# Performance work log

Measured on AMD Instinct MI355X. Metric: run time of the kernel, lower is better.

## Reference

```python
import jax, jax.numpy as jnp
import numpy as np

B, T, F, D, NL, V = 16, 1024, 80, 512, 3, 28


def _ln(x, g, b, eps=1e-5):
    m = jnp.mean(x, axis=-1, keepdims=True)
    v = jnp.mean((x - m) ** 2, axis=-1, keepdims=True)
    return (x - m) * jax.lax.rsqrt(v + eps) * g + b


def _sru_layer(x, W, wc, bias, g, beta):
    # x: [T, B, din]; W: [din, k*d] (k=4 when din != d, else k=3)
    d = wc.shape[0] // 2
    xn = _ln(x, g, beta)                       # layer_norm=True: LN on layer input
    U = jnp.einsum('tbi,ij->tbj', xn, W)       # [T, B, k*d]
    u0, u1, u2 = U[..., :d], U[..., d:2 * d], U[..., 2 * d:3 * d]
    xres = U[..., 3 * d:4 * d] if W.shape[1] == 4 * d else x  # highway input
    vf, vr = wc[:d], wc[d:]
    bf, br = bias[:d], bias[d:]

    def step(c, inp):
        a0, a1, a2, xr = inp
        f = jax.nn.sigmoid(a1 + vf * c + bf)
        r = jax.nn.sigmoid(a2 + vr * c + br)
        c2 = f * c + (1.0 - f) * a0
        h = r * c2 + (1.0 - r) * xr
        return c2, h

    c0 = jnp.zeros((x.shape[1], d), x.dtype)
    _, h = jax.lax.scan(step, c0, (u0, u1, u2, xres))
    return h


def _lstm_layer(x, wih, whh, bih, bhh):
    # x: [T, B, d]; torch gate order i, f, g, o
    d = whh.shape[1]
    gx = jnp.einsum('tbi,gi->tbg', x, wih) + bih + bhh  # precompute input gates

    def step(carry, gxt):
        h, c = carry
        gts = gxt + h @ whh.T
        i, f, gg, o = jnp.split(gts, 4, axis=-1)
        c2 = jax.nn.sigmoid(f) * c + jax.nn.sigmoid(i) * jnp.tanh(gg)
        h2 = jax.nn.sigmoid(o) * jnp.tanh(c2)
        return (h2, c2), h2

    nb = x.shape[1]
    init = (jnp.zeros((nb, d), x.dtype), jnp.zeros((nb, d), x.dtype))
    _, h = jax.lax.scan(step, init, gx)
    return h


def _forward(x, sru_w0, sru_wc0, sru_b0, sru_ln0_g, sru_ln0_b,
             sru_w, sru_wc, sru_b, sru_ln_g, sru_ln_b,
             lstm_ln_g, lstm_ln_b, lstm_wih, lstm_whh, lstm_bih, lstm_bhh,
             cls_ln_g, cls_ln_b, cls_w):
    h = jnp.transpose(x, (1, 0, 2))  # [T, B, F]
    h = _sru_layer(h, sru_w0, sru_wc0, sru_b0, sru_ln0_g, sru_ln0_b)
    for i in range(sru_w.shape[0]):  # 7 remaining SRU layers (8 total)
        h = _sru_layer(h, sru_w[i], sru_wc[i], sru_b[i], sru_ln_g[i], sru_ln_b[i])
    for i in range(lstm_wih.shape[0]):  # LSTM blocks: LN -> LSTM (dropout off, eval)
        hn = _ln(h, lstm_ln_g[i], lstm_ln_b[i])
        h = _lstm_layer(hn, lstm_wih[i], lstm_whh[i], lstm_bih[i], lstm_bhh[i])
    h = jnp.transpose(h, (1, 0, 2))  # [B, T, D]
    h = _ln(h, cls_ln_g, cls_ln_b)
    return h @ cls_w                 # [B, T, V+1]


def setup_inputs() -> dict:
    key = jax.random.key(0)
    ks = jax.random.split(key, 8)
    n = lambda k, s, sc: jax.random.normal(k, s, jnp.float32) * sc
    sF, sD = 1.0 / np.sqrt(F), 1.0 / np.sqrt(D)
    return {
        'x': n(ks[0], (B, T, F), 1.0),
        'sru_w0': n(ks[1], (F, 4 * D), sF),
        'sru_wc0': n(ks[2], (2 * D,), 0.1),
        'sru_b0': jnp.zeros((2 * D,), jnp.float32),
        'sru_ln0_g': jnp.ones((F,), jnp.float32),
        'sru_ln0_b': jnp.zeros((F,), jnp.float32),
        'sru_w': n(ks[3], (7, D, 3 * D), sD),
        'sru_wc': n(ks[4], (7, 2 * D), 0.1),
        'sru_b': jnp.zeros((7, 2 * D), jnp.float32),
        'sru_ln_g': jnp.ones((7, D), jnp.float32),
        'sru_ln_b': jnp.zeros((7, D), jnp.float32),
        'lstm_ln_g': jnp.ones((NL, D), jnp.float32),
        'lstm_ln_b': jnp.zeros((NL, D), jnp.float32),
        'lstm_wih': n(ks[5], (NL, 4 * D, D), sD),
        'lstm_whh': n(ks[6], (NL, 4 * D, D), sD),
        'lstm_bih': jnp.zeros((NL, 4 * D), jnp.float32),
        'lstm_bhh': jnp.zeros((NL, 4 * D), jnp.float32),
        'cls_ln_g': jnp.ones((D,), jnp.float32),
        'cls_ln_b': jnp.zeros((D,), jnp.float32),
        'cls_w': n(ks[7], (D, V + 1), sD),
    }


def reference(x, sru_w0, sru_wc0, sru_b0, sru_ln0_g, sru_ln0_b,
              sru_w, sru_wc, sru_b, sru_ln_g, sru_ln_b,
              lstm_ln_g, lstm_ln_b, lstm_wih, lstm_whh, lstm_bih, lstm_bhh,
              cls_ln_g, cls_ln_b, cls_w):
    return _forward(x, sru_w0, sru_wc0, sru_b0, sru_ln0_g, sru_ln0_b,
                    sru_w, sru_wc, sru_b, sru_ln_g, sru_ln_b,
                    lstm_ln_g, lstm_ln_b, lstm_wih, lstm_whh, lstm_bih, lstm_bhh,
                    cls_ln_g, cls_ln_b, cls_w)
```

## Files before the change

### kernel.cpp

```cpp
#include <hip/hip_runtime.h>
#include <stdint.h>
#include <stddef.h>

#define B_ 16
#define T_ 1024
#define F_ 80
#define D_ 512
#define M_ 16384
#define VO 29
#define SENT 0x7FC07FC0u
#define GPH 5

typedef float f32x4 __attribute__((ext_vector_type(4)));
typedef short s16x8 __attribute__((ext_vector_type(8)));
typedef unsigned short u16x8 __attribute__((ext_vector_type(8)));

static __device__ __forceinline__ unsigned short f2bf(float f) {
    union { float f; unsigned u; } v; v.f = f;
    unsigned r = v.u + 0x7FFFu + ((v.u >> 16) & 1u);
    return (unsigned short)(r >> 16);
}
static __device__ __forceinline__ float bf2f(unsigned short h) {
    union { unsigned u; float f; } v; v.u = ((unsigned)h) << 16; return v.f;
}
static __device__ __forceinline__ void split2(float v, unsigned short& hi, unsigned short& lo) {
    hi = f2bf(v);
    lo = f2bf(v - bf2f(hi));
}
static __device__ __forceinline__ float sigm(float x) {
    return 1.0f / (1.0f + __expf(-x));
}
static __device__ __forceinline__ float fast_tanh(float x) {
    return 1.0f - 2.0f / (__expf(2.0f * x) + 1.0f);
}
static __device__ __forceinline__ float wred(float v) {
    #pragma unroll
    for (int off = 1; off < 64; off <<= 1) v += __shfl_xor(v, off, 64);
    return v;
}
static __device__ __forceinline__ void stf_agent(float* p, float v) {
    union { float f; unsigned u; } c; c.f = v;
    __hip_atomic_store((unsigned*)p, c.u, __ATOMIC_RELAXED, __HIP_MEMORY_SCOPE_AGENT);
}
static __device__ __forceinline__ void gload16(const void* g, void* lds) {
    __builtin_amdgcn_global_load_lds(
        (const __attribute__((address_space(1))) void*)g,
        (__attribute__((address_space(3))) void*)lds, 16, 0, 0);
}

__global__ __launch_bounds__(256) void conv_w0(const float* __restrict__ W,
        unsigned short* __restrict__ Bh, unsigned short* __restrict__ Bl) {
    int gid = blockIdx.x * 256 + threadIdx.x;
    int n = gid / 96, k = gid - n * 96;
    float v = (k < 80) ? W[(size_t)k * 2048 + n] : 0.0f;
    unsigned short h, l; split2(v, h, l);
    Bh[gid] = h; Bl[gid] = l;
}
__global__ __launch_bounds__(256) void conv_sruw1(const float* __restrict__ W,
        unsigned short* __restrict__ Bh, unsigned short* __restrict__ Bl) {
    int gid = blockIdx.x * 256 + threadIdx.x;
    int n = gid >> 9, k = gid & 511;
    float v = W[(size_t)k * 1536 + n];
    unsigned short h, lo; split2(v, h, lo);
    Bh[gid] = h; Bl[gid] = lo;
}
__global__ __launch_bounds__(256) void conv_split(const float* __restrict__ W,
        unsigned short* __restrict__ Oh, unsigned short* __restrict__ Ol, int n) {
    int gid = blockIdx.x * 256 + threadIdx.x;
    if (gid < n) {
        unsigned short h, l; split2(W[gid], h, l);
        Oh[gid] = h; Ol[gid] = l;
    }
}
__global__ __launch_bounds__(256) void sent_fill(unsigned int* __restrict__ buf, int n) {
    int gid = blockIdx.x * 256 + threadIdx.x;
    if (gid < n)
        __hip_atomic_store(&buf[gid], SENT, __ATOMIC_RELAXED, __HIP_MEMORY_SCOPE_AGENT);
}
__global__ void zero_ctl(unsigned int* c) {
    if (threadIdx.x < 160)
        __hip_atomic_store(&c[threadIdx.x], 0u, __ATOMIC_RELAXED, __HIP_MEMORY_SCOPE_AGENT);
}

__global__ __launch_bounds__(256) void ln80_kernel(const float* __restrict__ x,
        const float* __restrict__ g, const float* __restrict__ bta,
        unsigned short* __restrict__ xh, unsigned short* __restrict__ xl) {
    int w = threadIdx.x >> 6, lane = threadIdx.x & 63;
    int row = blockIdx.x * 4 + w;
    int b = row & 15, t = row >> 4;
    const float* xr = x + ((size_t)b * T_ + t) * F_;
    float v0 = xr[lane];
    float v1 = (lane < 16) ? xr[64 + lane] : 0.0f;
    float mean = wred(v0 + v1) * (1.0f / 80.0f);
    float d0 = v0 - mean;
    float d1 = (lane < 16) ? (v1 - mean) : 0.0f;
    float var = wred(d0 * d0 + d1 * d1) * (1.0f / 80.0f);
    float rstd = rsqrtf(var + 1e-5f);
    float o0 = d0 * rstd * g[lane] + bta[lane];
    unsigned short h, l; split2(o0, h, l);
    xh[(size_t)row * 96 + lane] = h;
    xl[(size_t)row * 96 + lane] = l;
    if (lane < 32) {
        unsigned short hv = 0, lv = 0;
        if (lane < 16) {
            float o1 = d1 * rstd * g[64 + lane] + bta[64 + lane];
            split2(o1, hv, lv);
        }
        xh[(size_t)row * 96 + 64 + lane] = hv;
        xl[(size_t)row * 96 + 64 + lane] = lv;
    }
}

__global__ __launch_bounds__(256) void ln512_bf16(const float* __restrict__ hsrc,
        const float* __restrict__ g, const float* __restrict__ bta,
        unsigned short* __restrict__ oh, unsigned short* __restrict__ ol) {
    int w = threadIdx.x >> 6, lane = threadIdx.x & 63;
    size_t row = (size_t)blockIdx.x * 4 + w;
    const float* hr = hsrc + row * D_;
    float4 p0 = *(const float4*)(hr + lane * 8);
    float4 p1 = *(const float4*)(hr + lane * 8 + 4);
    float s = p0.x + p0.y + p0.z + p0.w + p1.x + p1.y + p1.z + p1.w;
    float mean = wred(s) * (1.0f / 512.0f);
    float d[8] = {p0.x - mean, p0.y - mean, p0.z - mean, p0.w - mean,
                  p1.x - mean, p1.y - mean, p1.z - mean, p1.w - mean};
    float q = 0.f;
    #pragma unroll
    for (int i = 0; i < 8; ++i) q += d[i] * d[i];
    float rstd = rsqrtf(wred(q) * (1.0f / 512.0f) + 1e-5f);
    const float* gp = g + lane * 8;
    const float* bp = bta + lane * 8;
    u16x8 vh, vl;
    #pragma unroll
    for (int i = 0; i < 8; ++i) {
        float o = d[i] * rstd * gp[i] + bp[i];
        unsigned short hh, ll; split2(o, hh, ll);
        vh[i] = hh; vl[i] = ll;
    }
    *(u16x8*)(oh + row * D_ + lane * 8) = vh;
    *(u16x8*)(ol + row * D_ + lane * 8) = vl;
}

__global__ __launch_bounds__(256) void ln512_f32(const float* __restrict__ hsrc,
        const float* __restrict__ g, const float* __restrict__ bta,
        float* __restrict__ o) {
    int w = threadIdx.x >> 6, lane = threadIdx.x & 63;
    size_t row = (size_t)blockIdx.x * 4 + w;
    const float* hr = hsrc + row * D_;
    float4 p0 = *(const float4*)(hr + lane * 8);
    float4 p1 = *(const float4*)(hr + lane * 8 + 4);
    float s = p0.x + p0.y + p0.z + p0.w + p1.x + p1.y + p1.z + p1.w;
    float mean = wred(s) * (1.0f / 512.0f);
    float d[8] = {p0.x - mean, p0.y - mean, p0.z - mean, p0.w - mean,
                  p1.x - mean, p1.y - mean, p1.z - mean, p1.w - mean};
    float q = 0.f;
    #pragma unroll
    for (int i = 0; i < 8; ++i) q += d[i] * d[i];
    float rstd = rsqrtf(wred(q) * (1.0f / 512.0f) + 1e-5f);
    const float* gp = g + lane * 8;
    const float* bp = bta + lane * 8;
    float* op = o + row * D_ + lane * 8;
    #pragma unroll
    for (int i = 0; i < 8; ++i) op[i] = d[i] * rstd * gp[i] + bp[i];
}

__global__ __launch_bounds__(256) void gemm_split(
        const unsigned short* __restrict__ Ah, const unsigned short* __restrict__ Al,
        const unsigned short* __restrict__ Bh, const unsigned short* __restrict__ Bl,
        float* __restrict__ C, int N, int Kp,
        const float* __restrict__ bias0, const float* __restrict__ bias1) {
    __shared__ __align__(16) unsigned short sAh[4096];
    __shared__ __align__(16) unsigned short sAl[4096];
    __shared__ __align__(16) unsigned short sBh[4096];
    __shared__ __align__(16) unsigned short sBl[4096];
    const int tid = threadIdx.x;
    const int wv = tid >> 6, lane = tid & 63;
    const int c_ = lane & 15, r_ = lane >> 4;
    const int wr = wv >> 1, wc = wv & 1;
    const int mBase = blockIdx.y * 128, nBase = blockIdx.x * 128;

    const int row0 = tid >> 2, row1 = 64 + row0;
    const int sp = tid & 3;
    const int x0 = (row0 & 3) ^ ((row0 >> 2) & 3);
    const int x1 = (row1 & 3) ^ ((row1 >> 2) & 3);
    const size_t gA0 = (size_t)(mBase + row0) * Kp + (size_t)((sp ^ x0) * 8);
    const size_t gA1 = (size_t)(mBase + row1) * Kp + (size_t)((sp ^ x1) * 8);
    const size_t gB0 = (size_t)(nBase + row0) * Kp + (size_t)((sp ^ x0) * 8);
    const size_t gB1 = (size_t)(nBase + row1) * Kp + (size_t)((sp ^ x1) * 8);
    const int ldsW = wv * 1024;

    int offA[4], offB[4];
    #pragma unroll
    for (int f = 0; f < 4; ++f) {
        int ra = wr * 64 + f * 16 + c_;
        int xa = (ra & 3) ^ ((ra >> 2) & 3);
        offA[f] = ra * 32 + ((r_ ^ xa) * 8);
        int rb = wc * 64 + f * 16 + c_;
        int xb = (rb & 3) ^ ((rb >> 2) & 3);
        offB[f] = rb * 32 + ((r_ ^ xb) * 8);
    }

    f32x4 acc[4][4] = {};
    for (int kt = 0; kt < Kp; kt += 32) {
        gload16(Ah + gA0 + kt, (char*)sAh + ldsW);
        gload16(Ah + gA1 + kt, (char*)sAh + 4096 + ldsW);
        gload16(Al + gA0 + kt, (char*)sAl + ldsW);
        gload16(Al + gA1 + kt, (char*)sAl + 4096 + ldsW);
        gload16(Bh + gB0 + kt, (char*)sBh + ldsW);
        gload16(Bh + gB1 + kt, (char*)sBh + 4096 + ldsW);
        gload16(Bl + gB0 + kt, (char*)sBl + ldsW);
        gload16(Bl + gB1 + kt, (char*)sBl + 4096 + ldsW);
        __syncthreads();
        s16x8 ah[4], al[4], bh[4], bl[4];
        #pragma unroll
        for (int f = 0; f < 4; ++f) {
            ah[f] = *(const s16x8*)&sAh[offA[f]];
            al[f] = *(const s16x8*)&sAl[offA[f]];
            bh[f] = *(const s16x8*)&sBh[offB[f]];
            bl[f] = *(const s16x8*)&sBl[offB[f]];
        }
        #pragma unroll
        for (int mf = 0; mf < 4; ++mf) {
            #pragma unroll
            for (int nf = 0; nf < 4; ++nf) {
                acc[mf][nf] = __builtin_amdgcn_mfma_f32_16x16x32_bf16(ah[mf], bh[nf], acc[mf][nf], 0, 0, 0);
                acc[mf][nf] = __builtin_amdgcn_mfma_f32_16x16x32_bf16(al[mf], bh[nf], acc[mf][nf], 0, 0, 0);
                acc[mf][nf] = __builtin_amdgcn_mfma_f32_16x16x32_bf16(ah[mf], bl[nf], acc[mf][nf], 0, 0, 0);
            }
        }
        __syncthreads();
    }
    #pragma unroll
    for (int mf = 0; mf < 4; ++mf) {
        #pragma unroll
        for (int r = 0; r < 4; ++r) {
            int m = mBase + wr * 64 + mf * 16 + r_ * 4 + r;
            float* crow = C + (size_t)m * N + nBase + wc * 64;
            #pragma unroll
            for (int nf = 0; nf < 4; ++nf) {
                int n = nBase + wc * 64 + nf * 16 + c_;
                float v = acc[mf][nf][r];
                if (bias0) v += bias0[n];
                if (bias1) v += bias1[n];
                crow[nf * 16 + c_] = v;
            }
        }
    }
}

__global__ __launch_bounds__(64) void sru_rec(const float* __restrict__ U, int NU,
        const float* __restrict__ xprev, const float* __restrict__ wc,
        const float* __restrict__ bias, float* __restrict__ hout) {
    int gid = blockIdx.x * 64 + threadIdx.x;
    int d = gid & (D_ - 1), b = gid >> 9;
    float vf = wc[d], vr = wc[D_ + d];
    float bf = bias[d], br = bias[D_ + d];
    const float* u0 = U + d;
    const float* u1 = U + D_ + d;
    const float* u2 = U + 2 * D_ + d;
    const float* xr;  size_t xstride;
    if (xprev) { xr = xprev + d; xstride = D_; }
    else       { xr = U + 3 * (size_t)D_ + d; xstride = (size_t)NU; }
    float* ho = hout + d;
    float c = 0.f;
    #pragma unroll 4
    for (int t = 0; t < T_; ++t) {
        size_t row = (size_t)(t * 16 + b);
        float a0 = u0[row * NU];
        float a1 = u1[row * NU];
        float a2 = u2[row * NU];
        float xv = xr[row * xstride];
        float f = sigm(a1 + vf * c + bf);
        float r = sigm(a2 + vr * c + br);
        c = f * c + (1.f - f) * a0;
        float h = r * c + (1.f - r) * xv;
        ho[row * D_] = h;
    }
}


template <int MODE>
static __device__ void lstm_role(int wg, const float* gxsrc,
        const unsigned short* Wh, const unsigned short* Wl,
        unsigned* ring, unsigned* myLprog,
        const unsigned* consCprog, float* hout) {
    __shared__ __align__(16) unsigned short hH[16][520];
    __shared__ float G[16][132];
    const int tid = threadIdx.x;
    const int w = tid >> 6, lane = tid & 63;
    const int c_ = lane & 15, r_ = lane >> 4;

    s16x8 bh0[16], bh1[16], bl0[16], bl1[16];
    {
        size_t R0 = (size_t)(w * 512 + wg * 32 + c_) * 512;
        size_t R1 = R0 + 16 * 512;
        #pragma unroll
        for (int ks = 0; ks < 16; ++ks) {
            bh0[ks] = *(const s16x8*)(Wh + R0 + ks * 32 + r_ * 8);
            bh1[ks] = *(const s16x8*)(Wh + R1 + ks * 32 + r_ * 8);
            bl0[ks] = *(const s16x8*)(Wl + R0 + ks * 32 + r_ * 8);
            bl1[ks] = *(const s16x8*)(Wl + R1 + ks * 32 + r_ * 8);
        }
    }
    for (int i = tid; i < 16 * 520; i += 256)
        ((unsigned short*)hH)[i] = 0;
    const int eb = tid >> 4;
    const int ed = (tid * 2) & 31;
    float cc0 = 0.f, cc1 = 0.f;
    const int col0 = w * 512 + wg * 32 + c_;
    const int hidx = (eb * 512 + wg * 32 + ed) >> 1;

    float gxv0[4], gxv1[4];
    if (MODE == 0) {
        #pragma unroll
        for (int r = 0; r < 4; ++r) {
            int bt = r_ * 4 + r;
            gxv0[r] = gxsrc[(size_t)bt * 2048 + col0];
            gxv1[r] = gxsrc[(size_t)bt * 2048 + col0 + 16];
        }
    } else {
        const float* gs = gxsrc;
        unsigned gv[8];
        unsigned gb = 0xFFu;
        while (true) {
            #pragma unroll
            for (int r = 0; r < 4; ++r) {
                int bt = r_ * 4 + r;
                if (gb & (1u << r))
                    gv[r] = __hip_atomic_load((const unsigned*)(gs + (size_t)bt * 2048 + col0),
                                              __ATOMIC_RELAXED, __HIP_MEMORY_SCOPE_AGENT);
                if (gb & (1u << (4 + r)))
                    gv[4 + r] = __hip_atomic_load((const unsigned*)(gs + (size_t)bt * 2048 + col0 + 16),
                                                  __ATOMIC_RELAXED, __HIP_MEMORY_SCOPE_AGENT);
            }
            unsigned nb = 0u;
            #pragma unroll
            for (int r = 0; r < 8; ++r)
                if ((gv[r] >> 16) == 0x7FC0u) nb |= 1u << r;
            gb = nb;
            if (!__any(gb != 0u)) break;
            __builtin_amdgcn_s_sleep(1);
        }
        #pragma unroll
        for (int r = 0; r < 4; ++r) {
            union { unsigned u; float f; } c0, c1;
            c0.u = gv[r]; c1.u = gv[4 + r];
            gxv0[r] = c0.f; gxv1[r] = c1.f;
        }
    }
    int pcur = 0, pnxt = 4096, pthr = 8192;
    __syncthreads();

    for (int t = 0; t < T_; ++t) {
        if (MODE == 1 && tid == 0)
            __hip_atomic_store(&myLprog[wg], (unsigned)t, __ATOMIC_RELAXED, __HIP_MEMORY_SCOPE_AGENT);
        if (consCprog) {
            int lim = t - 1;
            while (true) {
                int p = (int)__hip_atomic_load(&consCprog[lane & 31],
                                               __ATOMIC_RELAXED, __HIP_MEMORY_SCOPE_AGENT);
                if (__all(p >= lim)) break;
                __builtin_amdgcn_s_sleep(2);
            }
        }
        __hip_atomic_store(&ring[pnxt + hidx], SENT, __ATOMIC_RELAXED, __HIP_MEMORY_SCOPE_AGENT);
        f32x4 acc0 = {0.f, 0.f, 0.f, 0.f};
        f32x4 acc1 = {0.f, 0.f, 0.f, 0.f};
        #pragma unroll
        for (int ks = 0; ks < 16; ++ks) {
            s16x8 ah = *(const s16x8*)&hH[c_][ks * 32 + r_ * 8];
            acc0 = __builtin_amdgcn_mfma_f32_16x16x32_bf16(ah, bh0[ks], acc0, 0, 0, 0);
            acc1 = __builtin_amdgcn_mfma_f32_16x16x32_bf16(ah, bh1[ks], acc1, 0, 0, 0);
            acc0 = __builtin_amdgcn_mfma_f32_16x16x32_bf16(ah, bl0[ks], acc0, 0, 0, 0);
            acc1 = __builtin_amdgcn_mfma_f32_16x16x32_bf16(ah, bl1[ks], acc1, 0, 0, 0);
        }
        #pragma unroll
        for (int r = 0; r < 4; ++r) {
            int bt = r_ * 4 + r;
            G[bt][w * 32 + c_]      = acc0[r] + gxv0[r];
            G[bt][w * 32 + 16 + c_] = acc1[r] + gxv1[r];
        }
        __syncthreads();
        float iv0 = G[eb][ed],     fv0 = G[eb][32 + ed], gv0 = G[eb][64 + ed], ov0 = G[eb][96 + ed];
        float iv1 = G[eb][ed + 1], fv1 = G[eb][33 + ed], gv1 = G[eb][65 + ed], ov1 = G[eb][97 + ed];
        cc0 = sigm(fv0) * cc0 + sigm(iv0) * fast_tanh(gv0);
        cc1 = sigm(fv1) * cc1 + sigm(iv1) * fast_tanh(gv1);
        float h0 = sigm(ov0) * fast_tanh(cc0);
        float h1 = sigm(ov1) * fast_tanh(cc1);
        asm volatile("s_waitcnt vmcnt(0)" ::: "memory");
        unsigned packH = (unsigned)f2bf(h0) | ((unsigned)f2bf(h1) << 16);
        __hip_atomic_store(&ring[pcur + hidx], packH, __ATOMIC_RELAXED, __HIP_MEMORY_SCOPE_AGENT);
        if (hout) {
            size_t orow = (size_t)(t * 16 + eb) * D_ + wg * 32 + ed;
            hout[orow] = h0; hout[orow + 1] = h1;
        }
        if (t == T_ - 1) break;
        if (MODE == 0) {
            const float* gxr = gxsrc + (size_t)((t + 1) * 16) * 2048;
            #pragma unroll
            for (int r = 0; r < 4; ++r) {
                int bt = r_ * 4 + r;
                gxv0[r] = gxr[(size_t)bt * 2048 + col0];
                gxv1[r] = gxr[(size_t)bt * 2048 + col0 + 16];
            }
        } else {
            const float* gs = gxsrc + (size_t)((t + 1) % GPH) * 32768;
            unsigned gv[8];
            unsigned gb = 0xFFu;
            while (true) {
                #pragma unroll
                for (int r = 0; r < 4; ++r) {
                    int bt = r_ * 4 + r;
                    if (gb & (1u << r))
                        gv[r] = __hip_atomic_load((const unsigned*)(gs + (size_t)bt * 2048 + col0),
                                                  __ATOMIC_RELAXED, __HIP_MEMORY_SCOPE_AGENT);
                    if (gb & (1u << (4 + r)))
                        gv[4 + r] = __hip_atomic_load((const unsigned*)(gs + (size_t)bt * 2048 + col0 + 16),
                                                      __ATOMIC_RELAXED, __HIP_MEMORY_SCOPE_AGENT);
                }
                unsigned nb = 0u;
                #pragma unroll
                for (int r = 0; r < 8; ++r)
                    if ((gv[r] >> 16) == 0x7FC0u) nb |= 1u << r;
                gb = nb;
                if (!__any(gb != 0u)) break;
                __builtin_amdgcn_s_sleep(1);
            }
            #pragma unroll
            for (int r = 0; r < 4; ++r) {
                union { unsigned u; float f; } c0, c1;
                c0.u = gv[r]; c1.u = gv[4 + r];
                gxv0[r] = c0.f; gxv1[r] = c1.f;
            }
        }
        unsigned long long vh[8];
        unsigned badm = 0xFFu;
        while (true) {
            #pragma unroll
            for (int j = 0; j < 8; ++j) {
                int q = pcur + j * 512 + tid * 2;
                if (badm & (1u << j))
                    vh[j] = __hip_atomic_load((const unsigned long long*)&ring[q],
                                              __ATOMIC_RELAXED, __HIP_MEMORY_SCOPE_AGENT);
            }
            unsigned nb = 0u;
            #pragma unroll
            for (int j = 0; j < 8; ++j) {
                unsigned a0 = (unsigned)vh[j], a1 = (unsigned)(vh[j] >> 32);
                if (((a0 >> 16) == 0x7FC0u) || ((a1 >> 16) == 0x7FC0u)) nb |= 1u << j;
            }
            badm = nb;
            if (!__any(badm != 0u)) break;
            __builtin_amdgcn_s_sleep(1);
        }
        #pragma unroll
        for (int j = 0; j < 8; ++j) {
            int q = j * 512 + tid * 2;
            int bb = q >> 8, dd = (q & 255) * 2;
            *(unsigned long long*)&hH[bb][dd] = vh[j];
        }
        __syncthreads();
        int tmp = pcur; pcur = pnxt; pnxt = pthr; pthr = tmp;
    }
}

static __device__ void crew_role(int cid, const unsigned* srcring, float* gxr,
        unsigned* cprog, const unsigned* lprog,
        const unsigned short* WihHp, const unsigned short* WihLp,
        const float* g, const float* bta,
        const float* bihp, const float* bhhp) {
    __shared__ __align__(16) unsigned short xnH[16][520];
    __shared__ __align__(16) unsigned short xnL[16][520];
    const int tid = threadIdx.x;
    const int w = tid >> 6, lane = tid & 63;
    const int c_ = lane & 15, r_ = lane >> 4;
    const int col = cid * 64 + w * 16 + c_;
    const int rr = w * 4 + r_;

    s16x8 bfh[16], bfl[16];
    {
        const unsigned short* wrH = WihHp + (size_t)col * 512;
        const unsigned short* wrL = WihLp + (size_t)col * 512;
        #pragma unroll
        for (int ks = 0; ks < 16; ++ks) {
            bfh[ks] = *(const s16x8*)(wrH + ks * 32 + r_ * 8);
            bfl[ks] = *(const s16x8*)(wrL + ks * 32 + r_ * 8);
        }
    }
    const float bias = bihp[col] + bhhp[col];
    float lg[32], lb[32];
    #pragma unroll
    for (int j = 0; j < 32; ++j) { lg[j] = g[c_ * 32 + j]; lb[j] = bta[c_ * 32 + j]; }

    for (int t = 0; t < T_; ++t) {
        {
            int lim = t - 3;
            while (true) {
                int p = (int)__hip_atomic_load(&lprog[lane & 15],
                                               __ATOMIC_RELAXED, __HIP_MEMORY_SCOPE_AGENT);
                if (__all(p >= lim)) break;
                __builtin_amdgcn_s_sleep(2);
            }
        }
        {
            unsigned* rs = (unsigned*)(gxr + (size_t)((t + 1) % GPH) * 32768);
            #pragma unroll
            for (int r = 0; r < 4; ++r)
                __hip_atomic_store(&rs[(size_t)(r_ * 4 + r) * 2048 + col], SENT,
                                   __ATOMIC_RELAXED, __HIP_MEMORY_SCOPE_AGENT);
        }
        const unsigned* sb = srcring + (t % 3) * 4096;
        const int qi = rr * 256 + c_ * 16;
        unsigned long long vh[8];
        unsigned badm = 0xFFu;
        while (true) {
            #pragma unroll
            for (int j = 0; j < 8; ++j) {
                if (badm & (1u << j))
                    vh[j] = __hip_atomic_load((const unsigned long long*)&sb[qi + j * 2],
                                              __ATOMIC_RELAXED, __HIP_MEMORY_SCOPE_AGENT);
            }
            unsigned nb = 0u;
            #pragma unroll
            for (int j = 0; j < 8; ++j) {
                unsigned a0 = (unsigned)vh[j], a1 = (unsigned)(vh[j] >> 32);
                if (((a0 >> 16) == 0x7FC0u) || ((a1 >> 16) == 0x7FC0u)) nb |= 1u << j;
            }
            badm = nb;
            if (!__any(badm != 0u)) break;
            __builtin_amdgcn_s_sleep(1);
        }
        float x[32];
        #pragma unroll
        for (int k = 0; k < 8; ++k) {
            unsigned ah = (unsigned)vh[k], bh = (unsigned)(vh[k] >> 32);
            x[4 * k + 0] = bf2f((unsigned short)ah);
            x[4 * k + 1] = bf2f((unsigned short)(ah >> 16));
            x[4 * k + 2] = bf2f((unsigned short)bh);
            x[4 * k + 3] = bf2f((unsigned short)(bh >> 16));
        }
        float s = 0.f;
        #pragma unroll
        for (int j = 0; j < 32; ++j) s += x[j];
        #pragma unroll
        for (int m = 1; m < 16; m <<= 1) s += __shfl_xor(s, m, 64);
        float mean = s * (1.0f / 512.0f);
        float q = 0.f;
        #pragma unroll
        for (int j = 0; j < 32; ++j) { float d = x[j] - mean; q += d * d; }
        #pragma unroll
        for (int m = 1; m < 16; m <<= 1) q += __shfl_xor(q, m, 64);
        float rstd = rsqrtf(q * (1.0f / 512.0f) + 1e-5f);
        u16x8 ph[4], pl[4];
        #pragma unroll
        for (int j = 0; j < 32; ++j) {
            float o = (x[j] - mean) * rstd * lg[j] + lb[j];
            unsigned short hh, ll; split2(o, hh, ll);
            ph[j >> 3][j & 7] = (unsigned short)hh;
            pl[j >> 3][j & 7] = (unsigned short)ll;
        }
        #pragma unroll
        for (int jj = 0; jj < 4; ++jj) {
            *(u16x8*)&xnH[rr][c_ * 32 + jj * 8] = ph[jj];
            *(u16x8*)&xnL[rr][c_ * 32 + jj * 8] = pl[jj];
        }
        __syncthreads();
        if (tid == 0)
            __hip_atomic_store(&cprog[cid], (unsigned)(t + 1), __ATOMIC_RELAXED, __HIP_MEMORY_SCOPE_AGENT);
        f32x4 acc = {bias, bias, bias, bias};
        #pragma unroll
        for (int ks = 0; ks < 16; ++ks) {
            s16x8 axh = *(const s16x8*)&xnH[c_][ks * 32 + r_ * 8];
            s16x8 axl = *(const s16x8*)&xnL[c_][ks * 32 + r_ * 8];
            acc = __builtin_amdgcn_mfma_f32_16x16x32_bf16(axh, bfh[ks], acc, 0, 0, 0);
            acc = __builtin_amdgcn_mfma_f32_16x16x32_bf16(axl, bfh[ks], acc, 0, 0, 0);
            acc = __builtin_amdgcn_mfma_f32_16x16x32_bf16(axh, bfl[ks], acc, 0, 0, 0);
        }
        asm volatile("s_waitcnt vmcnt(0)" ::: "memory");
        float* gs = gxr + (size_t)(t % GPH) * 32768;
        #pragma unroll
        for (int r = 0; r < 4; ++r)
            stf_agent(gs + (size_t)(r_ * 4 + r) * 2048 + col, acc[r]);
        __syncthreads();
    }
}

__global__ __launch_bounds__(256, 1) void lstm_pipe(
        const float* __restrict__ gx0,
        const unsigned short* __restrict__ WhhH, const unsigned short* __restrict__ WhhL,
        const unsigned short* __restrict__ WihH, const unsigned short* __restrict__ WihL,
        const float* __restrict__ lng, const float* __restrict__ lnb,
        const float* __restrict__ bih, const float* __restrict__ bhh,
        float* __restrict__ hout,
        unsigned* __restrict__ rings,
        float* __restrict__ gxr,
        unsigned* __restrict__ ctl) {
    const int bid = blockIdx.x;
    const size_t WSL = (size_t)2048 * 512;
    const int RNG = 3 * 4096;
    if (bid < 16) {
        lstm_role<0>(bid, gx0, WhhH, WhhL, rings,
                     nullptr, ctl + 96, nullptr);
    } else if (bid < 32) {
        lstm_role<1>(bid - 16, gxr, WhhH + WSL, WhhL + WSL, rings + RNG,
                     ctl + 64, ctl + 128, nullptr);
    } else if (bid < 48) {
        lstm_role<1>(bid - 32, gxr + (size_t)GPH * 32768, WhhH + 2 * WSL, WhhL + 2 * WSL,
                     rings + 2 * RNG, ctl + 80, nullptr, hout);
    } else if (bid < 80) {
        crew_role(bid - 48, rings, gxr, ctl + 96, ctl + 64,
                  WihH, WihL, lng + 512, lnb + 512, bih + 2048, bhh + 2048);
    } else {
        crew_role(bid - 80, rings + RNG, gxr + (size_t)GPH * 32768, ctl + 128, ctl + 80,
                  WihH + WSL, WihL + WSL, lng + 1024, lnb + 1024, bih + 4096, bhh + 4096);
    }
}

__global__ __launch_bounds__(256) void cls_gemm(const float* __restrict__ xn,
        const float* __restrict__ wcls, float* __restrict__ out) {
    __shared__ float wl[512][32];
    int tid = threadIdx.x;
    for (int idx = tid; idx < 512 * VO; idx += 256) {
        int k = idx / VO, v = idx - k * VO;
        wl[k][v] = wcls[idx];
    }
    __syncthreads();
    int r8 = tid >> 5, v = tid & 31;
    int row = blockIdx.x * 8 + r8;
    if (v >= VO) return;
    const float* xr = xn + (size_t)row * D_;
    float acc = 0.f;
    #pragma unroll 8
    for (int k = 0; k < 512; ++k) acc += xr[k] * wl[k][v];
    int b = row & 15, t = row >> 4;
    out[((size_t)b * T_ + t) * VO + v] = acc;
}

extern "C" void kernel_launch(void* const* d_in, const int* in_sizes, int n_in,
                              void* d_out, int out_size, void* d_ws, size_t ws_size,
                              hipStream_t stream) {
    const float* x        = (const float*)d_in[0];
    const float* sru_w0   = (const float*)d_in[1];
    const float* sru_wc0  = (const float*)d_in[2];
    const float* sru_b0   = (const float*)d_in[3];
    const float* sru_ln0g = (const float*)d_in[4];
    const float* sru_ln0b = (const float*)d_in[5];
    const float* sru_w    = (const float*)d_in[6];
    const float* sru_wc   = (const float*)d_in[7];
    const float* sru_b    = (const float*)d_in[8];
    const float* sru_lng  = (const float*)d_in[9];
    const float* sru_lnb  = (const float*)d_in[10];
    const float* lstm_lng = (const float*)d_in[11];
    const float* lstm_lnb = (const float*)d_in[12];
    const float* lstm_wih = (const float*)d_in[13];
    const float* lstm_whh = (const float*)d_in[14];
    const float* lstm_bih = (const float*)d_in[15];
    const float* lstm_bhh = (const float*)d_in[16];
    const float* cls_lng  = (const float*)d_in[17];
    const float* cls_lnb  = (const float*)d_in[18];
    const float* cls_w    = (const float*)d_in[19];
    float* out = (float*)d_out;

    char* ws = (char*)d_ws;
    size_t off = 0;
    auto alloc = [&](size_t bytes) -> void* {
        off = (off + 255) & ~(size_t)255;
        void* p = ws + off;
        off += bytes;
        return p;
    };
    float* U             = (float*)alloc((size_t)M_ * 1536 * 4);
    float* hP            = (float*)alloc((size_t)M_ * D_ * 4);
    float* hQ            = (float*)alloc((size_t)M_ * D_ * 4);
    unsigned short* xnh  = (unsigned short*)alloc((size_t)M_ * D_ * 2);
    unsigned short* xnl  = (unsigned short*)alloc((size_t)M_ * D_ * 2);
    unsigned short* w0h  = (unsigned short*)alloc((size_t)2048 * 96 * 2);
    unsigned short* w0l  = (unsigned short*)alloc((size_t)2048 * 96 * 2);
    unsigned short* swh  = (unsigned short*)alloc((size_t)1536 * 512 * 2);
    unsigned short* swl  = (unsigned short*)alloc((size_t)1536 * 512 * 2);
    unsigned short* wihh = (unsigned short*)alloc((size_t)2048 * 512 * 2);
    unsigned short* wihl = (unsigned short*)alloc((size_t)2048 * 512 * 2);
    unsigned short* whh3h = (unsigned short*)alloc((size_t)3 * 2048 * 512 * 2);
    unsigned short* whh3l = (unsigned short*)alloc((size_t)3 * 2048 * 512 * 2);
    unsigned short* wih2h = (unsigned short*)alloc((size_t)2 * 2048 * 512 * 2);
    unsigned short* wih2l = (unsigned short*)alloc((size_t)2 * 2048 * 512 * 2);
    unsigned* rings = (unsigned*)swh;
    float*    gxr   = (float*)swl;
    unsigned* ctl   = (unsigned*)(((char*)swh) + 3 * 3 * 4096 * 4);
    float* gx = U;

    hipLaunchKernelGGL(conv_w0, dim3(768), dim3(256), 0, stream, sru_w0, w0h, w0l);

    hipLaunchKernelGGL(ln80_kernel, dim3(4096), dim3(256), 0, stream, x, sru_ln0g, sru_ln0b, xnh, xnl);
    hipLaunchKernelGGL(gemm_split, dim3(2048 / 128, M_ / 128), dim3(256), 0, stream,
                       xnh, xnl, w0h, w0l, gx, 2048, 96, (const float*)nullptr, (const float*)nullptr);
    hipLaunchKernelGGL(sru_rec, dim3(128), dim3(64), 0, stream,
                       gx, 2048, (const float*)nullptr, sru_wc0, sru_b0, hQ);

    float* hcur = hQ; float* hnxt = hP;
    for (int l = 0; l < 7; ++l) {
        hipLaunchKernelGGL(conv_sruw1, dim3(3072), dim3(256), 0, stream,
                           sru_w + (size_t)l * 512 * 1536, swh, swl);
        hipLaunchKernelGGL(ln512_bf16, dim3(4096), dim3(256), 0, stream,
                           hcur, sru_lng + (size_t)l * 512, sru_lnb + (size_t)l * 512, xnh, xnl);
        hipLaunchKernelGGL(gemm_split, dim3(1536 / 128, M_ / 128), dim3(256), 0, stream,
                           xnh, xnl, swh, swl, U, 1536, 512,
                           (const float*)nullptr, (const float*)nullptr);
        hipLaunchKernelGGL(sru_rec, dim3(128), dim3(64), 0, stream,
                           U, 1536, hcur, sru_wc + (size_t)l * 1024, sru_b + (size_t)l * 1024, hnxt);
        float* tmp = hcur; hcur = hnxt; hnxt = tmp;
    }

    hipLaunchKernelGGL(conv_split, dim3(12288), dim3(256), 0, stream,
                       lstm_whh, whh3h, whh3l, 3 * 2048 * 512);
    hipLaunchKernelGGL(conv_split, dim3(8192), dim3(256), 0, stream,
                       lstm_wih + (size_t)2048 * 512, wih2h, wih2l, 2 * 2048 * 512);
    hipLaunchKernelGGL(conv_split, dim3(4096), dim3(256), 0, stream,
                       lstm_wih, wihh, wihl, 2048 * 512);
    hipLaunchKernelGGL(ln512_bf16, dim3(4096), dim3(256), 0, stream,
                       hcur, lstm_lng, lstm_lnb, xnh, xnl);
    hipLaunchKernelGGL(gemm_split, dim3(2048 / 128, M_ / 128), dim3(256), 0, stream,
                       xnh, xnl, wihh, wihl, gx, 2048, 512, lstm_bih, lstm_bhh);
    hipLaunchKernelGGL(sent_fill, dim3(144), dim3(256), 0, stream, rings, 3 * 3 * 4096);
    hipLaunchKernelGGL(sent_fill, dim3(1280), dim3(256), 0, stream, (unsigned*)gxr, 2 * GPH * 32768);
    hipLaunchKernelGGL(zero_ctl, dim3(1), dim3(256), 0, stream, ctl);

    hipLaunchKernelGGL(lstm_pipe, dim3(112), dim3(256), 0, stream,
                       gx, whh3h, whh3l, wih2h, wih2l,
                       lstm_lng, lstm_lnb, lstm_bih, lstm_bhh,
                       hQ, rings, gxr, ctl);

    hipLaunchKernelGGL(ln512_f32, dim3(4096), dim3(256), 0, stream, hQ, cls_lng, cls_lnb, (float*)U);
    hipLaunchKernelGGL(cls_gemm, dim3(2048), dim3(256), 0, stream, (const float*)U, cls_w, out);
}
```

Measured before the change: 7.999 ms.

## Overlap weight conversion with SRU recurrence and drop A-low GEMM term

Weight bf16 hi/lo splitting for the next SRU layer and for the LSTM weights now runs in extra blocks of the SRU recurrence kernel. These conversions fill otherwise idle CUs while the 128 latency-bound recurrence blocks run, and several separate conversion launches go away. The SRU-layer GEMMs for layers 1-7 use a 2-term split (the A-low term is dropped), which removes one MFMA per tile and the A-low load and store. The three init kernels are merged into one launch. Dropping the activation low part lowers SRU GEMM precision. Conversion blocks also compete with the recurrence blocks for memory bandwidth.

```diff
diff --git a/kernel.cpp b/kernel.cpp
--- a/kernel.cpp
+++ b/kernel.cpp
@@ -56,30 +56,17 @@
     unsigned short h, l; split2(v, h, l);
     Bh[gid] = h; Bl[gid] = l;
 }
-__global__ __launch_bounds__(256) void conv_sruw1(const float* __restrict__ W,
-        unsigned short* __restrict__ Bh, unsigned short* __restrict__ Bl) {
-    int gid = blockIdx.x * 256 + threadIdx.x;
-    int n = gid >> 9, k = gid & 511;
-    float v = W[(size_t)k * 1536 + n];
-    unsigned short h, lo; split2(v, h, lo);
-    Bh[gid] = h; Bl[gid] = lo;
-}
-__global__ __launch_bounds__(256) void conv_split(const float* __restrict__ W,
-        unsigned short* __restrict__ Oh, unsigned short* __restrict__ Ol, int n) {
-    int gid = blockIdx.x * 256 + threadIdx.x;
-    if (gid < n) {
-        unsigned short h, l; split2(W[gid], h, l);
-        Oh[gid] = h; Ol[gid] = l;
-    }
-}
-__global__ __launch_bounds__(256) void sent_fill(unsigned int* __restrict__ buf, int n) {
-    int gid = blockIdx.x * 256 + threadIdx.x;
-    if (gid < n)
-        __hip_atomic_store(&buf[gid], SENT, __ATOMIC_RELAXED, __HIP_MEMORY_SCOPE_AGENT);
-}
-__global__ void zero_ctl(unsigned int* c) {
-    if (threadIdx.x < 160)
-        __hip_atomic_store(&c[threadIdx.x], 0u, __ATOMIC_RELAXED, __HIP_MEMORY_SCOPE_AGENT);
+__global__ __launch_bounds__(256) void pipe_init(unsigned* __restrict__ rings, int nring,
+        unsigned* __restrict__ gxr, int ngx, unsigned* __restrict__ ctl) {
+    int total = nring + ngx + 160;
+    for (int i = blockIdx.x * 256 + threadIdx.x; i < total; i += gridDim.x * 256) {
+        if (i < nring)
+            __hip_atomic_store(&rings[i], SENT, __ATOMIC_RELAXED, __HIP_MEMORY_SCOPE_AGENT);
+        else if (i < nring + ngx)
+            __hip_atomic_store(&gxr[i - nring], SENT, __ATOMIC_RELAXED, __HIP_MEMORY_SCOPE_AGENT);
+        else
+            __hip_atomic_store(&ctl[i - nring - ngx], 0u, __ATOMIC_RELAXED, __HIP_MEMORY_SCOPE_AGENT);
+    }
 }
 
 __global__ __launch_bounds__(256) void ln80_kernel(const float* __restrict__ x,
@@ -111,6 +98,7 @@
     }
 }
 
+template <bool LO>
 __global__ __launch_bounds__(256) void ln512_bf16(const float* __restrict__ hsrc,
         const float* __restrict__ g, const float* __restrict__ bta,
         unsigned short* __restrict__ oh, unsigned short* __restrict__ ol) {
@@ -137,7 +125,7 @@
         vh[i] = hh; vl[i] = ll;
     }
     *(u16x8*)(oh + row * D_ + lane * 8) = vh;
-    *(u16x8*)(ol + row * D_ + lane * 8) = vl;
+    if (LO) *(u16x8*)(ol + row * D_ + lane * 8) = vl;
 }
 
 __global__ __launch_bounds__(256) void ln512_f32(const float* __restrict__ hsrc,
@@ -163,13 +151,14 @@
     for (int i = 0; i < 8; ++i) op[i] = d[i] * rstd * gp[i] + bp[i];
 }
 
-__global__ __launch_bounds__(256) void gemm_split(
+template <int TERMS>
+__global__ __launch_bounds__(256) void gemm_split_t(
         const unsigned short* __restrict__ Ah, const unsigned short* __restrict__ Al,
         const unsigned short* __restrict__ Bh, const unsigned short* __restrict__ Bl,
         float* __restrict__ C, int N, int Kp,
         const float* __restrict__ bias0, const float* __restrict__ bias1) {
     __shared__ __align__(16) unsigned short sAh[4096];
-    __shared__ __align__(16) unsigned short sAl[4096];
+    __shared__ __align__(16) unsigned short sAl[TERMS == 3 ? 4096 : 16];
     __shared__ __align__(16) unsigned short sBh[4096];
     __shared__ __align__(16) unsigned short sBl[4096];
     const int tid = threadIdx.x;
@@ -203,8 +192,10 @@
     for (int kt = 0; kt < Kp; kt += 32) {
         gload16(Ah + gA0 + kt, (char*)sAh + ldsW);
         gload16(Ah + gA1 + kt, (char*)sAh + 4096 + ldsW);
-        gload16(Al + gA0 + kt, (char*)sAl + ldsW);
-        gload16(Al + gA1 + kt, (char*)sAl + 4096 + ldsW);
+        if constexpr (TERMS == 3) {
+            gload16(Al + gA0 + kt, (char*)sAl + ldsW);
+            gload16(Al + gA1 + kt, (char*)sAl + 4096 + ldsW);
+        }
         gload16(Bh + gB0 + kt, (char*)sBh + ldsW);
         gload16(Bh + gB1 + kt, (char*)sBh + 4096 + ldsW);
         gload16(Bl + gB0 + kt, (char*)sBl + ldsW);
@@ -214,7 +205,7 @@
         #pragma unroll
         for (int f = 0; f < 4; ++f) {
             ah[f] = *(const s16x8*)&sAh[offA[f]];
-            al[f] = *(const s16x8*)&sAl[offA[f]];
+            if constexpr (TERMS == 3) al[f] = *(const s16x8*)&sAl[offA[f]];
             bh[f] = *(const s16x8*)&sBh[offB[f]];
             bl[f] = *(const s16x8*)&sBl[offB[f]];
         }
@@ -223,7 +214,8 @@
             #pragma unroll
             for (int nf = 0; nf < 4; ++nf) {
                 acc[mf][nf] = __builtin_amdgcn_mfma_f32_16x16x32_bf16(ah[mf], bh[nf], acc[mf][nf], 0, 0, 0);
-                acc[mf][nf] = __builtin_amdgcn_mfma_f32_16x16x32_bf16(al[mf], bh[nf], acc[mf][nf], 0, 0, 0);
+                if constexpr (TERMS == 3)
+                    acc[mf][nf] = __builtin_amdgcn_mfma_f32_16x16x32_bf16(al[mf], bh[nf], acc[mf][nf], 0, 0, 0);
                 acc[mf][nf] = __builtin_amdgcn_mfma_f32_16x16x32_bf16(ah[mf], bl[nf], acc[mf][nf], 0, 0, 0);
             }
         }
@@ -247,33 +239,62 @@
     }
 }
 
-__global__ __launch_bounds__(64) void sru_rec(const float* __restrict__ U, int NU,
+__global__ __launch_bounds__(64) void sru_fused(const float* __restrict__ U, int NU,
         const float* __restrict__ xprev, const float* __restrict__ wc,
-        const float* __restrict__ bias, float* __restrict__ hout) {
-    int gid = blockIdx.x * 64 + threadIdx.x;
-    int d = gid & (D_ - 1), b = gid >> 9;
-    float vf = wc[d], vr = wc[D_ + d];
-    float bf = bias[d], br = bias[D_ + d];
-    const float* u0 = U + d;
-    const float* u1 = U + D_ + d;
-    const float* u2 = U + 2 * D_ + d;
-    const float* xr;  size_t xstride;
-    if (xprev) { xr = xprev + d; xstride = D_; }
-    else       { xr = U + 3 * (size_t)D_ + d; xstride = (size_t)NU; }
-    float* ho = hout + d;
-    float c = 0.f;
-    #pragma unroll 4
-    for (int t = 0; t < T_; ++t) {
-        size_t row = (size_t)(t * 16 + b);
-        float a0 = u0[row * NU];
-        float a1 = u1[row * NU];
-        float a2 = u2[row * NU];
-        float xv = xr[row * xstride];
-        float f = sigm(a1 + vf * c + bf);
-        float r = sigm(a2 + vr * c + br);
-        c = f * c + (1.f - f) * a0;
-        float h = r * c + (1.f - r) * xv;
-        ho[row * D_] = h;
+        const float* __restrict__ bias, float* __restrict__ hout,
+        const float* __restrict__ sA, unsigned short* __restrict__ dAh,
+        unsigned short* __restrict__ dAl, int nA,
+        const float* __restrict__ sB, unsigned short* __restrict__ dBh,
+        unsigned short* __restrict__ dBl, int nB,
+        const float* __restrict__ sC, unsigned short* __restrict__ dCh,
+        unsigned short* __restrict__ dCl, int nC,
+        const float* __restrict__ sD, unsigned short* __restrict__ dDh,
+        unsigned short* __restrict__ dDl, int nD) {
+    const int bid = blockIdx.x;
+    if (bid < 128) {
+        int gid = bid * 64 + threadIdx.x;
+        int d = gid & (D_ - 1), b = gid >> 9;
+        float vf = wc[d], vr = wc[D_ + d];
+        float bf = bias[d], br = bias[D_ + d];
+        const float* u0 = U + d;
+        const float* u1 = U + D_ + d;
+        const float* u2 = U + 2 * D_ + d;
+        const float* xr;  size_t xstride;
+        if (xprev) { xr = xprev + d; xstride = D_; }
+        else       { xr = U + 3 * (size_t)D_ + d; xstride = (size_t)NU; }
+        float* ho = hout + d;
+        float c = 0.f;
+        #pragma unroll 4
+        for (int t = 0; t < T_; ++t) {
+            size_t row = (size_t)(t * 16 + b);
+            float a0 = u0[row * NU];
+            float a1 = u1[row * NU];
+            float a2 = u2[row * NU];
+            float xv = xr[row * xstride];
+            float f = sigm(a1 + vf * c + bf);
+            float r = sigm(a2 + vr * c + br);
+            c = f * c + (1.f - f) * a0;
+            float h = r * c + (1.f - r) * xv;
+            ho[row * D_] = h;
+        }
+    } else {
+        const int total = nA + nB + nC + nD;
+        const int stride = (2176 - 128) * 64;
+        for (int idx = (bid - 128) * 64 + threadIdx.x; idx < total; idx += stride) {
+            float v; unsigned short *oh, *ol; int o;
+            if (idx < nA) {
+                int n = idx >> 9, k = idx & 511;
+                v = sA[(size_t)k * 1536 + n]; oh = dAh; ol = dAl; o = idx;
+            } else if (idx < nA + nB) {
+                o = idx - nA; v = sB[o]; oh = dBh; ol = dBl;
+            } else if (idx < nA + nB + nC) {
+                o = idx - nA - nB; v = sC[o]; oh = dCh; ol = dCl;
+            } else {
+                o = idx - nA - nB - nC; v = sD[o]; oh = dDh; ol = dDl;
+            }
+            unsigned short h, l; split2(v, h, l);
+            oh[o] = h; ol[o] = l;
+        }
     }
 }
 
@@ -688,41 +709,44 @@
     unsigned* ctl   = (unsigned*)(((char*)swh) + 3 * 3 * 4096 * 4);
     float* gx = U;
 
+    const int WSL = 2048 * 512;
+    const int NSW = 1536 * 512;
+
     hipLaunchKernelGGL(conv_w0, dim3(768), dim3(256), 0, stream, sru_w0, w0h, w0l);
 
     hipLaunchKernelGGL(ln80_kernel, dim3(4096), dim3(256), 0, stream, x, sru_ln0g, sru_ln0b, xnh, xnl);
-    hipLaunchKernelGGL(gemm_split, dim3(2048 / 128, M_ / 128), dim3(256), 0, stream,
+    hipLaunchKernelGGL(gemm_split_t<3>, dim3(2048 / 128, M_ / 128), dim3(256), 0, stream,
                        xnh, xnl, w0h, w0l, gx, 2048, 96, (const float*)nullptr, (const float*)nullptr);
-    hipLaunchKernelGGL(sru_rec, dim3(128), dim3(64), 0, stream,
-                       gx, 2048, (const float*)nullptr, sru_wc0, sru_b0, hQ);
+    hipLaunchKernelGGL(sru_fused, dim3(2176), dim3(64), 0, stream,
+                       gx, 2048, (const float*)nullptr, sru_wc0, sru_b0, hQ,
+                       sru_w, swh, swl, NSW,
+                       lstm_whh, whh3h, whh3l, 3 * WSL,
+                       lstm_wih, wihh, wihl, WSL,
+                       lstm_wih + (size_t)WSL, wih2h, wih2l, 2 * WSL);
 
     float* hcur = hQ; float* hnxt = hP;
     for (int l = 0; l < 7; ++l) {
-        hipLaunchKernelGGL(conv_sruw1, dim3(3072), dim3(256), 0, stream,
-                           sru_w + (size_t)l * 512 * 1536, swh, swl);
-        hipLaunchKernelGGL(ln512_bf16, dim3(4096), dim3(256), 0, stream,
+        hipLaunchKernelGGL(ln512_bf16<false>, dim3(4096), dim3(256), 0, stream,
                            hcur, sru_lng + (size_t)l * 512, sru_lnb + (size_t)l * 512, xnh, xnl);
-        hipLaunchKernelGGL(gemm_split, dim3(1536 / 128, M_ / 128), dim3(256), 0, stream,
-                           xnh, xnl, swh, swl, U, 1536, 512,
+        hipLaunchKernelGGL(gemm_split_t<2>, dim3(1536 / 128, M_ / 128), dim3(256), 0, stream,
+                           xnh, xnh, swh, swl, U, 1536, 512,
                            (const float*)nullptr, (const float*)nullptr);
-        hipLaunchKernelGGL(sru_rec, dim3(128), dim3(64), 0, stream,
-                           U, 1536, hcur, sru_wc + (size_t)l * 1024, sru_b + (size_t)l * 1024, hnxt);
+        int nA = (l < 6) ? NSW : 0;
+        hipLaunchKernelGGL(sru_fused, dim3(2176), dim3(64), 0, stream,
+                           U, 1536, hcur, sru_wc + (size_t)l * 1024, sru_b + (size_t)l * 1024, hnxt,
+                           sru_w + (size_t)(l + 1) * NSW, swh, swl, nA,
+                           lstm_whh, whh3h, whh3l, 0,
+                           lstm_wih, wihh, wihl, 0,
+                           lstm_wih, wih2h, wih2l, 0);
         float* tmp = hcur; hcur = hnxt; hnxt = tmp;
     }
 
-    hipLaunchKernelGGL(conv_split, dim3(12288), dim3(256), 0, stream,
-                       lstm_whh, whh3h, whh3l, 3 * 2048 * 512);
-    hipLaunchKernelGGL(conv_split, dim3(8192), dim3(256), 0, stream,
-                       lstm_wih + (size_t)2048 * 512, wih2h, wih2l, 2 * 2048 * 512);
-    hipLaunchKernelGGL(conv_split, dim3(4096), dim3(256), 0, stream,
-                       lstm_wih, wihh, wihl, 2048 * 512);
-    hipLaunchKernelGGL(ln512_bf16, dim3(4096), dim3(256), 0, stream,
+    hipLaunchKernelGGL(ln512_bf16<true>, dim3(4096), dim3(256), 0, stream,
                        hcur, lstm_lng, lstm_lnb, xnh, xnl);
-    hipLaunchKernelGGL(gemm_split, dim3(2048 / 128, M_ / 128), dim3(256), 0, stream,
+    hipLaunchKernelGGL(gemm_split_t<3>, dim3(2048 / 128, M_ / 128), dim3(256), 0, stream,
                        xnh, xnl, wihh, wihl, gx, 2048, 512, lstm_bih, lstm_bhh);
-    hipLaunchKernelGGL(sent_fill, dim3(144), dim3(256), 0, stream, rings, 3 * 3 * 4096);
-    hipLaunchKernelGGL(sent_fill, dim3(1280), dim3(256), 0, stream, (unsigned*)gxr, 2 * GPH * 32768);
-    hipLaunchKernelGGL(zero_ctl, dim3(1), dim3(256), 0, stream, ctl);
+    hipLaunchKernelGGL(pipe_init, dim3(1024), dim3(256), 0, stream,
+                       rings, 3 * 3 * 4096, (unsigned*)gxr, 2 * GPH * 32768, ctl);
 
     hipLaunchKernelGGL(lstm_pipe, dim3(112), dim3(256), 0, stream,
                        gx, whh3h, whh3l, wih2h, wih2l,
```

Measured after the change: 7.836 ms, median of 2. 1.02x faster.
